# Optimization experiments

Hardware: AMD Instinct MI355X
Metric: run time of the kernel (lower is better)

Reference implementation:

```python
import jax, jax.numpy as jnp
import numpy as np

B, S, D, H, E = 4, 2048, 512, 8, 4  # batch, seq, embed, heads, expand
HD = D // H


def setup_inputs() -> dict:
    key = jax.random.key(0)
    ks = jax.random.split(key, 9)
    s = lambda k, shape, fan: jax.random.normal(k, shape, jnp.float32) * (fan ** -0.5)
    return {
        "x": jax.random.normal(ks[0], (B, S, D), jnp.float32),
        "Wq": s(ks[1], (D, D), D),
        "Wk": s(ks[2], (D, D), D),
        "Wv": s(ks[3], (D, D), D),
        "Wo": s(ks[4], (D, D), D),
        "W1": s(ks[5], (D, D * E), D),
        "b1": jnp.zeros((D * E,), jnp.float32),
        "W2": s(ks[6], (D * E, D), D * E),
        "b2": jnp.zeros((D,), jnp.float32),
    }


def _encoder_layer(x, Wq, Wk, Wv, Wo, W1, b1, W2, b2):
    # NOTE: source computes InstanceNorm1d twice but discards both results -> no-ops.
    scale = D ** -0.25  # applied to BOTH q and k (net 1/sqrt(embed_dim))
    q = (x @ Wq).reshape(B, S, H, HD).transpose(0, 2, 1, 3) * scale  # [B,H,S,hd]
    k = (x @ Wk).reshape(B, S, H, HD).transpose(0, 2, 1, 3) * scale
    v = (x @ Wv).reshape(B, S, H, HD).transpose(0, 2, 1, 3)
    scores = jnp.einsum('bhqd,bhkd->bhqk', q, k)  # [B,H,S,S]
    attn = jax.nn.softmax(scores, axis=-1)
    o = jnp.einsum('bhqk,bhkd->bhqd', attn, v)  # [B,H,S,hd]
    o = o.transpose(0, 2, 1, 3).reshape(B, S, D)
    x = o @ Wo + x  # residual 1
    h = jax.nn.gelu(x @ W1 + b1, approximate=True)  # torch GELU(approximate='tanh')
    return h @ W2 + b2 + x  # residual 2 (dropout=0, eval)


def reference(x, Wq, Wk, Wv, Wo, W1, b1, W2, b2):
    return _encoder_layer(x, Wq, Wk, Wv, Wo, W1, b1, W2, b2)
```

## Files before the change

kernel.cpp:

```cpp
#include <hip/hip_runtime.h>
#include <hip/hip_bf16.h>


typedef __bf16 bf16;
typedef __attribute__((ext_vector_type(8))) __bf16 bf16x8;
typedef __attribute__((ext_vector_type(4))) __bf16 bf16x4;
typedef __attribute__((ext_vector_type(4))) float f32x4;
typedef __attribute__((ext_vector_type(16))) float f32x16;
typedef __attribute__((ext_vector_type(2))) unsigned int u32x2;
typedef __attribute__((ext_vector_type(4))) unsigned int u32x4;

#define LOG2E 1.4426950408889634f
#define SCORE_SCALE 0.044194173824159216f
#define SCALE_L2E (SCORE_SCALE * LOG2E)

#if __has_builtin(__builtin_amdgcn_exp2f)
#define EXP2(x) __builtin_amdgcn_exp2f(x)
#else
#define EXP2(x) exp2f(x)
#endif

__device__ __forceinline__ void gl_lds16(const bf16* g, bf16* l) {
  __builtin_amdgcn_global_load_lds(
      (const __attribute__((address_space(1))) unsigned int*)g,
      (__attribute__((address_space(3))) unsigned int*)l, 16, 0, 0);
}

template <int N>
__device__ __forceinline__ void wait_vm_barrier() {
  if constexpr (N == 0)
    asm volatile("s_waitcnt vmcnt(0)\ns_barrier" ::: "memory");
  else if constexpr (N == 2)
    asm volatile("s_waitcnt vmcnt(2)\ns_barrier" ::: "memory");
  else if constexpr (N == 3)
    asm volatile("s_waitcnt vmcnt(3)\ns_barrier" ::: "memory");
  else if constexpr (N == 4)
    asm volatile("s_waitcnt vmcnt(4)\ns_barrier" ::: "memory");
  else if constexpr (N == 8)
    asm volatile("s_waitcnt vmcnt(8)\ns_barrier" ::: "memory");
}

__device__ __forceinline__ float gelu_tanh(float x) {
  float u = 0.7978845608028654f * (x + 0.044715f * x * x * x);
  float e = EXP2(u * (2.0f * LOG2E));
  float th = 1.0f - 2.0f / (e + 1.0f);
  return 0.5f * x * (1.0f + th);
}

__device__ __forceinline__ f32x4 mfma_bf16(bf16x8 a, bf16x8 b, f32x4 c) {
  return __builtin_amdgcn_mfma_f32_16x16x32_bf16(a, b, c, 0, 0, 0);
}
__device__ __forceinline__ f32x16 mfma32x16(bf16x8 a, bf16x8 b, f32x16 c) {
  return __builtin_amdgcn_mfma_f32_32x32x16_bf16(a, b, c, 0, 0, 0);
}

__device__ __forceinline__ void plswap(unsigned int& a, unsigned int& b) {
  asm volatile("v_permlane32_swap_b32 %0, %1" : "+v"(a), "+v"(b));
}

__device__ __forceinline__ void xcd_remap(int& bx, int& by) {
  const int gx = gridDim.x;
  const int nwg = gx * gridDim.y;
  const int lin = blockIdx.y * gx + blockIdx.x;
  const int id = (lin & 7) * (nwg >> 3) + (lin >> 3);
  bx = id % gx;
  by = id / gx;
}

template <int MODE, typename OutT, int TN>
__global__ __launch_bounds__(256, 2) void gemm_bt(
    const bf16* __restrict__ A, const bf16* __restrict__ Bt,
    OutT* __restrict__ C, const float* __restrict__ bias,
    const float* __restrict__ resf, const bf16* __restrict__ resb,
    bf16* __restrict__ vt, int M, int N, int K) {
  constexpr int MI = (TN == 128) ? 4 : 2;
  constexpr int NBUF = (TN == 128) ? 2 : 3;
  __shared__ __align__(16) bf16 sA[NBUF][128 * 32];
  __shared__ __align__(16) bf16 sB[NBUF][TN * 32];
  const int tid = threadIdx.x;
  const int lane = tid & 63;
  const int quad = lane >> 4, lc = lane & 15;
  const int wave = tid >> 6;
  const int wr = (TN == 128) ? (wave >> 1) : wave;
  const int wc = (TN == 128) ? (wave & 1) : 0;
  int bxs, bys;
  xcd_remap(bxs, bys);
  const int m0 = bys * 128, n0 = bxs * TN;

  const int srow = tid >> 2;
  const int kc = (tid & 3) * 8;
  const bf16* Ag1 = A + (size_t)(m0 + srow) * K + kc;
  const bf16* Ag2 = A + (size_t)(m0 + 64 + srow) * K + kc;
  const bf16* Bg1 = Bt + (size_t)(n0 + srow) * K + kc;
  const bf16* Bg2 = Bt + (size_t)(n0 + 64 + srow) * K + kc;
  const int o1 = tid * 8, o2 = (tid + 256) * 8;

  f32x4 acc[MI][4];
#pragma unroll
  for (int mi = 0; mi < MI; ++mi)
#pragma unroll
    for (int ni = 0; ni < 4; ++ni) acc[mi][ni] = (f32x4){0.f, 0.f, 0.f, 0.f};

  const int kIters = K >> 5;

  if constexpr (TN == 128) {
    gl_lds16(Ag1, sA[0] + o1);
    gl_lds16(Ag2, sA[0] + o2);
    gl_lds16(Bg1, sB[0] + o1);
    gl_lds16(Bg2, sB[0] + o2);
    Ag1 += 32; Ag2 += 32; Bg1 += 32; Bg2 += 32;

    for (int kt = 0; kt < kIters; ++kt) {
      __syncthreads();
      const bf16* cA = sA[kt & 1];
      const bf16* cB = sB[kt & 1];
      if (kt + 1 < kIters) {
        bf16* nA = sA[(kt + 1) & 1];
        bf16* nB = sB[(kt + 1) & 1];
        gl_lds16(Ag1, nA + o1);
        gl_lds16(Ag2, nA + o2);
        gl_lds16(Bg1, nB + o1);
        gl_lds16(Bg2, nB + o2);
        Ag1 += 32; Ag2 += 32; Bg1 += 32; Bg2 += 32;
      }
      bf16x8 af[MI], bfm[4];
#pragma unroll
      for (int i = 0; i < MI; ++i)
        af[i] = *(const bf16x8*)(cA +
                                 ((wr * 64 + i * 16 + lc) * 32 + quad * 8));
#pragma unroll
      for (int i = 0; i < 4; ++i)
        bfm[i] =
            *(const bf16x8*)(cB + ((wc * 64 + i * 16 + lc) * 32 + quad * 8));
#pragma unroll
      for (int mi = 0; mi < MI; ++mi)
#pragma unroll
        for (int ni = 0; ni < 4; ++ni)
          acc[mi][ni] = mfma_bf16(af[mi], bfm[ni], acc[mi][ni]);
    }
  } else {
    auto stage = [&](int t) {
      bf16* a = sA[t % 3];
      bf16* bb = sB[t % 3];
      gl_lds16(Ag1 + t * 32, a + o1);
      gl_lds16(Ag2 + t * 32, a + o2);
      gl_lds16(Bg1 + t * 32, bb + o1);
    };
    stage(0);
    stage(1);
    for (int kt = 0; kt < kIters; ++kt) {
      if (kt + 1 < kIters)
        wait_vm_barrier<3>();
      else
        wait_vm_barrier<0>();
      if (kt + 2 < kIters) stage(kt + 2);
      const bf16* cA = sA[kt % 3];
      const bf16* cB = sB[kt % 3];
      bf16x8 af[MI], bfm[4];
#pragma unroll
      for (int i = 0; i < MI; ++i)
        af[i] = *(const bf16x8*)(cA +
                                 ((wr * 32 + i * 16 + lc) * 32 + quad * 8));
#pragma unroll
      for (int i = 0; i < 4; ++i)
        bfm[i] = *(const bf16x8*)(cB + ((i * 16 + lc) * 32 + quad * 8));
#pragma unroll
      for (int mi = 0; mi < MI; ++mi)
#pragma unroll
        for (int ni = 0; ni < 4; ++ni)
          acc[mi][ni] = mfma_bf16(af[mi], bfm[ni], acc[mi][ni]);
    }
  }

  if constexpr (MODE == 0) {
    if (n0 >= 1024) {
#pragma unroll
      for (int mi = 0; mi < MI; ++mi) {
        const int row0 = m0 + wr * (16 * MI) + mi * 16 + quad * 4;
        const int bb = row0 >> 11, s0 = row0 & 2047;
#pragma unroll
        for (int ni = 0; ni < 4; ++ni) {
          const int col = n0 + wc * 64 + ni * 16 + lc;
          const int hh = (col >> 6) & 7, d = col & 63;
          bf16x4 pb;
#pragma unroll
          for (int r = 0; r < 4; ++r) pb[r] = (bf16)acc[mi][ni][r];
          *(bf16x4*)(vt + ((size_t)((bb * 8 + hh) * 64 + d)) * 2048 + s0) = pb;
        }
      }
      return;
    }
  }
  const float qscale = (MODE == 0 && n0 < 512) ? SCALE_L2E : 1.0f;
#pragma unroll
  for (int mi = 0; mi < MI; ++mi) {
#pragma unroll
    for (int r = 0; r < 4; ++r) {
      const int row = m0 + wr * (16 * MI) + mi * 16 + quad * 4 + r;
#pragma unroll
      for (int ni = 0; ni < 4; ++ni) {
        const int col = n0 + wc * 64 + ni * 16 + lc;
        const size_t idx = (size_t)row * N + col;
        float v = acc[mi][ni][r];
        if (MODE == 0) v *= qscale;
        if (MODE == 1) v += resf[idx];
        if (MODE == 2) v = gelu_tanh(v + bias[col]);
        if (MODE == 3) v += bias[col] + (float)resb[idx];
        C[idx] = (OutT)v;
      }
    }
  }
}

__global__ __launch_bounds__(512, 2) void gemm256v2(
    const bf16* __restrict__ A, const bf16* __restrict__ Bt,
    bf16* __restrict__ C, const float* __restrict__ bias, int M, int N,
    int K) {
  __shared__ __align__(16) bf16 sA[4][8192];
  __shared__ __align__(16) bf16 sB[4][8192];
  const int tid = threadIdx.x;
  const int lane = tid & 63;
  const int quad = lane >> 4, lc = lane & 15;
  const int w8 = tid >> 6;
  const int wm = w8 >> 2, wn = w8 & 3;
  int bxs, bys;
  xcd_remap(bxs, bys);
  const int m0 = bys * 256, n0 = bxs * 256;

  const int srow0 = tid >> 2;
  const int cpos = tid & 3;

  f32x4 acc[8][4];
#pragma unroll
  for (int mi = 0; mi < 8; ++mi)
#pragma unroll
    for (int ni = 0; ni < 4; ++ni) acc[mi][ni] = (f32x4){0.f, 0.f, 0.f, 0.f};

  auto stage = [&](int t) {
    bf16* a = sA[t & 3];
    bf16* bb = sB[t & 3];
    const int k0 = t * 32;
#pragma unroll
    for (int c = 0; c < 2; ++c) {
      const int row = c * 128 + srow0;
      const int sc = (cpos ^ (row & 3)) * 8;
      gl_lds16(A + (size_t)(m0 + row) * K + k0 + sc, a + c * 4096 + tid * 8);
      gl_lds16(Bt + (size_t)(n0 + row) * K + k0 + sc, bb + c * 4096 + tid * 8);
    }
  };

  const int kIters = K >> 5;
  stage(0);
  stage(1);
  stage(2);

  const int cxq = (quad ^ (lc & 3)) << 3;

  for (int kt = 0; kt < kIters; ++kt) {
    const int left = kIters - 1 - kt;
    if (left >= 2)
      wait_vm_barrier<8>();
    else if (left == 1)
      wait_vm_barrier<4>();
    else
      wait_vm_barrier<0>();
    if (kt + 3 < kIters) stage(kt + 3);
    const bf16* cA = sA[kt & 3];
    const bf16* cB = sB[kt & 3];

    bf16x8 af[8], bfm[4];
#pragma unroll
    for (int i = 0; i < 4; ++i)
      af[i] = *(const bf16x8*)(cA + (wm * 128 + i * 16 + lc) * 32 + cxq);
#pragma unroll
    for (int j = 0; j < 4; ++j)
      bfm[j] = *(const bf16x8*)(cB + (wn * 64 + j * 16 + lc) * 32 + cxq);
    __builtin_amdgcn_s_barrier();
    __builtin_amdgcn_s_setprio(1);
#pragma unroll
    for (int mi = 0; mi < 4; ++mi)
#pragma unroll
      for (int ni = 0; ni < 4; ++ni)
        acc[mi][ni] = mfma_bf16(af[mi], bfm[ni], acc[mi][ni]);
    __builtin_amdgcn_s_setprio(0);
#pragma unroll
    for (int i = 4; i < 8; ++i)
      af[i] = *(const bf16x8*)(cA + (wm * 128 + i * 16 + lc) * 32 + cxq);
    __builtin_amdgcn_s_barrier();
    __builtin_amdgcn_s_setprio(1);
#pragma unroll
    for (int mi = 4; mi < 8; ++mi)
#pragma unroll
      for (int ni = 0; ni < 4; ++ni)
        acc[mi][ni] = mfma_bf16(af[mi], bfm[ni], acc[mi][ni]);
    __builtin_amdgcn_s_setprio(0);
  }

#pragma unroll
  for (int mi = 0; mi < 8; ++mi) {
#pragma unroll
    for (int r = 0; r < 4; ++r) {
      const int row = m0 + wm * 128 + mi * 16 + quad * 4 + r;
#pragma unroll
      for (int ni = 0; ni < 4; ++ni) {
        const int col = n0 + wn * 64 + ni * 16 + lc;
        C[(size_t)row * N + col] = (bf16)gelu_tanh(acc[mi][ni][r] + bias[col]);
      }
    }
  }
}

__global__ __launch_bounds__(256, 4) void flash_attn(
    const bf16* __restrict__ QKV, const bf16* __restrict__ Vt,
    float* __restrict__ O0, float* __restrict__ O1, float* __restrict__ Rp) {
  const int tid = threadIdx.x;
  const int lane = tid & 63, wave = tid >> 6;
  const int lo5 = lane & 31, hi = lane >> 5;
  const int lin = blockIdx.y * 16 + blockIdx.x;
  const int xcd = lin & 7, slot = lin >> 3;
  const int bh = xcd * 4 + (slot >> 4);
  const int qt = slot & 15;
  const int b = bh >> 3, h = bh & 7;
  const int q0 = qt * 128 + wave * 32;
  const int half = blockIdx.z;
  const int t0 = half << 4;

  __shared__ __align__(16) bf16 sK[3][4096];
  __shared__ __align__(16) bf16 sV[2][4096];

  const bf16* Qrow = QKV + (size_t)(b * 2048 + q0 + lo5) * 1536 + h * 64;
  bf16x8 qf[4];
#pragma unroll
  for (int i = 0; i < 4; ++i) qf[i] = *(const bf16x8*)(Qrow + i * 16 + hi * 8);

  const int colsw = (((lane & 7) ^ (lane >> 3)) << 3);
  const bf16* Kg0 = QKV + (size_t)b * 2048 * 1536 + 512 + (size_t)h * 64 +
                    (size_t)(wave * 16 + (lane >> 3)) * 1536 + colsw;
  const bf16* Vg0 = Vt + (size_t)bh * 64 * 2048 +
                    (size_t)(wave * 16 + (lane >> 3)) * 2048 + colsw;
  const int stag = wave * 1024;
  const int m7 = lo5 & 7;

  f32x16 oacc[2];
  oacc[0] = (f32x16)(0.f);
  oacc[1] = (f32x16)(0.f);
  float rs0 = 0.f, rs1 = 0.f, rs2 = 0.f, rs3 = 0.f;

  auto stageK = [&](int lt) {
    bf16* dk = sK[lt % 3] + stag;
    const int g = t0 + lt;
    gl_lds16(Kg0 + (size_t)g * 64 * 1536, dk);
    gl_lds16(Kg0 + (size_t)(g * 64 + 8) * 1536, dk + 512);
  };
  auto stageV = [&](int lt) {
    bf16* dv = sV[lt & 1] + stag;
    const int g = t0 + lt;
    gl_lds16(Vg0 + g * 64, dv);
    gl_lds16(Vg0 + g * 64 + 8 * 2048, dv + 512);
  };
  stageK(0);
  stageV(0);
  stageK(1);

  bf16x8 paw[4];

  auto softmax = [&](const f32x16& st, int hl) {
    unsigned int q32[4][2];
#pragma unroll
    for (int g = 0; g < 4; ++g) {
      bf16x4 pb;
      float p0 = EXP2(st[4 * g + 0]);
      float p1 = EXP2(st[4 * g + 1]);
      float p2 = EXP2(st[4 * g + 2]);
      float p3 = EXP2(st[4 * g + 3]);
      rs0 += p0; rs1 += p1; rs2 += p2; rs3 += p3;
      pb[0] = (bf16)p0; pb[1] = (bf16)p1; pb[2] = (bf16)p2; pb[3] = (bf16)p3;
      u32x2 w2 = __builtin_bit_cast(u32x2, pb);
      q32[g][0] = w2[0];
      q32[g][1] = w2[1];
    }
#pragma unroll
    for (int t = 0; t < 2; ++t) {
      unsigned int a0 = q32[2 * t][0], a1 = q32[2 * t][1];
      unsigned int b0 = q32[2 * t + 1][0], b1 = q32[2 * t + 1][1];
      plswap(a0, b0);
      plswap(a1, b1);
      u32x4 f = {a0, a1, b0, b1};
      paw[hl * 2 + t] = __builtin_bit_cast(bf16x8, f);
    }
  };

  for (int kt = 0; kt < 16; ++kt) {
    if (kt == 15)
      wait_vm_barrier<0>();
    else
      wait_vm_barrier<2>();
    if (kt + 1 < 16) stageV(kt + 1);
    if (kt + 2 < 16) stageK(kt + 2);
    const bf16* cK = sK[kt % 3];
    const bf16* cV = sV[kt & 1];

    bf16x8 vf[2][4], kf[2][4];
#pragma unroll
    for (int dh = 0; dh < 2; ++dh) {
      const int Rd = dh * 32 + lo5;
#pragma unroll
      for (int w = 0; w < 4; ++w)
        vf[dh][w] =
            *(const bf16x8*)(cV + Rd * 64 + (((2 * w + hi) ^ m7) << 3));
    }
#pragma unroll
    for (int hl = 0; hl < 2; ++hl) {
      const int R = hl * 32 + lo5;
#pragma unroll
      for (int i = 0; i < 4; ++i)
        kf[hl][i] =
            *(const bf16x8*)(cK + R * 64 + (((2 * i + hi) ^ m7) << 3));
    }

    f32x16 st0 = (f32x16)(0.f), st1 = (f32x16)(0.f);
    __builtin_amdgcn_s_setprio(1);
#pragma unroll
    for (int i = 0; i < 4; ++i) {
      st0 = mfma32x16(kf[0][i], qf[i], st0);
      st1 = mfma32x16(kf[1][i], qf[i], st1);
    }
    __builtin_amdgcn_s_setprio(0);

    softmax(st0, 0);
#pragma unroll
    for (int w = 0; w < 2; ++w) {
      oacc[0] = mfma32x16(paw[w], vf[0][w], oacc[0]);
      oacc[1] = mfma32x16(paw[w], vf[1][w], oacc[1]);
    }
    softmax(st1, 1);
    __builtin_amdgcn_s_setprio(1);
#pragma unroll
    for (int w = 2; w < 4; ++w) {
      oacc[0] = mfma32x16(paw[w], vf[0][w], oacc[0]);
      oacc[1] = mfma32x16(paw[w], vf[1][w], oacc[1]);
    }
    __builtin_amdgcn_s_setprio(0);
  }

  float rsum = (rs0 + rs1) + (rs2 + rs3);
  rsum += __shfl_xor(rsum, 32, 64);
  float* Op = half ? O1 : O0;
  const size_t obase = (size_t)(b * 2048 + q0) * 512 + h * 64;
#pragma unroll
  for (int r = 0; r < 16; ++r) {
    const int qloc = (r & 3) + 8 * (r >> 2) + 4 * hi;
#pragma unroll
    for (int dh = 0; dh < 2; ++dh)
      Op[obase + (size_t)qloc * 512 + dh * 32 + lo5] = oacc[dh][r];
  }
  if (hi == 0)
    Rp[(size_t)(half * 8 + h) * 8192 + b * 2048 + q0 + lo5] = rsum;
}

__global__ __launch_bounds__(256) void combine(
    const float* __restrict__ O0, const float* __restrict__ O1,
    const float* __restrict__ Rp, bf16* __restrict__ attn) {
  const int i4 = blockIdx.x * 256 + threadIdx.x;
  const int row = i4 >> 7;
  const int col = (i4 & 127) * 4;
  const int h = col >> 6;
  const float inv =
      1.0f / (Rp[(size_t)h * 8192 + row] + Rp[(size_t)(8 + h) * 8192 + row]);
  const float4 a = ((const float4*)O0)[i4];
  const float4 b = ((const float4*)O1)[i4];
  bf16x4 o;
  o[0] = (bf16)((a.x + b.x) * inv);
  o[1] = (bf16)((a.y + b.y) * inv);
  o[2] = (bf16)((a.z + b.z) * inv);
  o[3] = (bf16)((a.w + b.w) * inv);
  *(bf16x4*)(attn + (size_t)i4 * 4) = o;
}

__global__ __launch_bounds__(256) void prep(
    const float* __restrict__ x, const float* __restrict__ Wq,
    const float* __restrict__ Wk, const float* __restrict__ Wv,
    const float* __restrict__ Wo, const float* __restrict__ W1,
    const float* __restrict__ W2, bf16* __restrict__ xb,
    bf16* __restrict__ WqkvT, bf16* __restrict__ WoT, bf16* __restrict__ W1T,
    bf16* __restrict__ W2T) {
  const int bid = blockIdx.x;
  if (bid < 4096) {
    const size_t i = ((size_t)bid * 256 + threadIdx.x) * 4;
    const float4 v = *(const float4*)(x + i);
    bf16x4 o;
    o[0] = (bf16)v.x; o[1] = (bf16)v.y; o[2] = (bf16)v.z; o[3] = (bf16)v.w;
    *(bf16x4*)(xb + i) = o;
    return;
  }
  const int t = bid - 4096;
  const float* in;
  bf16* out;
  int in_ld, out_ld, bx, by;
  if (t < 1024) {
    const int q = t >> 8, r = t & 255;
    bx = r & 15; by = r >> 4; in_ld = 512; out_ld = 512;
    in = (q == 0) ? Wq : (q == 1) ? Wk : (q == 2) ? Wv : Wo;
    out = (q == 0) ? WqkvT
          : (q == 1) ? WqkvT + 512 * 512
          : (q == 2) ? WqkvT + 2 * 512 * 512
                     : WoT;
  } else if (t < 2048) {
    const int r = t - 1024;
    bx = r & 63; by = r >> 6; in_ld = 2048; out_ld = 512;
    in = W1; out = W1T;
  } else {
    const int r = t - 2048;
    bx = r & 15; by = r >> 4; in_ld = 512; out_ld = 2048;
    in = W2; out = W2T;
  }
  __shared__ __align__(16) bf16 tl[32][33];
  const int tx = threadIdx.x & 31, ty = threadIdx.x >> 5;
  const int n0 = bx * 32, k0 = by * 32;
#pragma unroll
  for (int i = 0; i < 4; ++i)
    tl[ty + 8 * i][tx] = (bf16)in[(size_t)(k0 + ty + 8 * i) * in_ld + n0 + tx];
  __syncthreads();
#pragma unroll
  for (int i = 0; i < 4; ++i)
    out[(size_t)(n0 + ty + 8 * i) * out_ld + k0 + tx] = tl[tx][ty + 8 * i];
}

extern "C" void kernel_launch(void* const* d_in, const int* in_sizes, int n_in,
                              void* d_out, int out_size, void* d_ws,
                              size_t ws_size, hipStream_t stream) {
  const float* x = (const float*)d_in[0];
  const float* Wq = (const float*)d_in[1];
  const float* Wk = (const float*)d_in[2];
  const float* Wv = (const float*)d_in[3];
  const float* Wo = (const float*)d_in[4];
  const float* W1 = (const float*)d_in[5];
  const float* b1 = (const float*)d_in[6];
  const float* W2 = (const float*)d_in[7];
  const float* b2 = (const float*)d_in[8];
  float* out = (float*)d_out;

  char* ws = (char*)d_ws;
  size_t off = 0;
  auto alloc = [&](size_t bytes) {
    char* p = ws + off;
    off += (bytes + 255) & ~(size_t)255;
    return p;
  };
  bf16* WqkvT = (bf16*)alloc(1536ULL * 512 * 2);
  bf16* WoT = (bf16*)alloc(512ULL * 512 * 2);
  bf16* W1T = (bf16*)alloc(2048ULL * 512 * 2);
  bf16* W2T = (bf16*)alloc(512ULL * 2048 * 2);
  bf16* xb = (bf16*)alloc(8192ULL * 512 * 2);
  bf16* QKV = (bf16*)alloc(8192ULL * 1536 * 2);
  bf16* Vt = (bf16*)alloc(32ULL * 64 * 2048 * 2);
  bf16* attn = (bf16*)alloc(8192ULL * 512 * 2);
  float* Opart1 = (float*)alloc(8192ULL * 512 * 4);
  float* Rpart = (float*)alloc(2ULL * 8 * 8192 * 4);
  float* Opart0 = out;
  bf16* x2 = xb;
  bf16* hbuf = QKV;

  const dim3 tb(256);
  prep<<<dim3(7168), tb, 0, stream>>>(x, Wq, Wk, Wv, Wo, W1, W2, xb, WqkvT,
                                      WoT, W1T, W2T);
  gemm_bt<0, bf16, 128><<<dim3(12, 64), tb, 0, stream>>>(
      xb, WqkvT, QKV, nullptr, nullptr, nullptr, Vt, 8192, 1536, 512);
  flash_attn<<<dim3(16, 32, 2), tb, 0, stream>>>(QKV, Vt, Opart0, Opart1,
                                                 Rpart);
  combine<<<dim3(4096), tb, 0, stream>>>(Opart0, Opart1, Rpart, attn);
  gemm_bt<1, bf16, 64><<<dim3(8, 64), tb, 0, stream>>>(
      attn, WoT, x2, nullptr, x, nullptr, nullptr, 8192, 512, 512);
  gemm256v2<<<dim3(8, 32), dim3(512), 0, stream>>>(x2, W1T, hbuf, b1, 8192,
                                                   2048, 512);
  gemm_bt<3, float, 64><<<dim3(8, 64), tb, 0, stream>>>(
      hbuf, W2T, out, b2, nullptr, x2, nullptr, 8192, 512, 2048);
}
```

Baseline: 285.0 us.

## Merge split-KV attention halves into one block and reduce through LDS

```diff
diff --git a/kernel.cpp b/kernel.cpp
--- a/kernel.cpp
+++ b/kernel.cpp
@@ -310,23 +310,23 @@
   }
 }
 
-__global__ __launch_bounds__(256, 4) void flash_attn(
+__global__ __launch_bounds__(512, 2) void flash_attn(
     const bf16* __restrict__ QKV, const bf16* __restrict__ Vt,
-    float* __restrict__ O0, float* __restrict__ O1, float* __restrict__ Rp) {
+    bf16* __restrict__ O) {
   const int tid = threadIdx.x;
   const int lane = tid & 63, wave = tid >> 6;
+  const int hs = wave >> 2, w4 = wave & 3;
   const int lo5 = lane & 31, hi = lane >> 5;
   const int lin = blockIdx.y * 16 + blockIdx.x;
   const int xcd = lin & 7, slot = lin >> 3;
   const int bh = xcd * 4 + (slot >> 4);
   const int qt = slot & 15;
   const int b = bh >> 3, h = bh & 7;
-  const int q0 = qt * 128 + wave * 32;
-  const int half = blockIdx.z;
-  const int t0 = half << 4;
-
-  __shared__ __align__(16) bf16 sK[3][4096];
-  __shared__ __align__(16) bf16 sV[2][4096];
+  const int q0 = qt * 128 + w4 * 32;
+  const int t0 = hs << 4;
+
+  __shared__ __align__(16) bf16 sK[2][3][4096];
+  __shared__ __align__(16) bf16 sV[2][2][4096];
 
   const bf16* Qrow = QKV + (size_t)(b * 2048 + q0 + lo5) * 1536 + h * 64;
   bf16x8 qf[4];
@@ -335,10 +335,10 @@
 
   const int colsw = (((lane & 7) ^ (lane >> 3)) << 3);
   const bf16* Kg0 = QKV + (size_t)b * 2048 * 1536 + 512 + (size_t)h * 64 +
-                    (size_t)(wave * 16 + (lane >> 3)) * 1536 + colsw;
+                    (size_t)(w4 * 16 + (lane >> 3)) * 1536 + colsw;
   const bf16* Vg0 = Vt + (size_t)bh * 64 * 2048 +
-                    (size_t)(wave * 16 + (lane >> 3)) * 2048 + colsw;
-  const int stag = wave * 1024;
+                    (size_t)(w4 * 16 + (lane >> 3)) * 2048 + colsw;
+  const int stag = w4 * 1024;
   const int m7 = lo5 & 7;
 
   f32x16 oacc[2];
@@ -347,13 +347,13 @@
   float rs0 = 0.f, rs1 = 0.f, rs2 = 0.f, rs3 = 0.f;
 
   auto stageK = [&](int lt) {
-    bf16* dk = sK[lt % 3] + stag;
+    bf16* dk = sK[hs][lt % 3] + stag;
     const int g = t0 + lt;
     gl_lds16(Kg0 + (size_t)g * 64 * 1536, dk);
     gl_lds16(Kg0 + (size_t)(g * 64 + 8) * 1536, dk + 512);
   };
   auto stageV = [&](int lt) {
-    bf16* dv = sV[lt & 1] + stag;
+    bf16* dv = sV[hs][lt & 1] + stag;
     const int g = t0 + lt;
     gl_lds16(Vg0 + g * 64, dv);
     gl_lds16(Vg0 + g * 64 + 8 * 2048, dv + 512);
@@ -397,8 +397,8 @@
       wait_vm_barrier<2>();
     if (kt + 1 < 16) stageV(kt + 1);
     if (kt + 2 < 16) stageK(kt + 2);
-    const bf16* cK = sK[kt % 3];
-    const bf16* cV = sV[kt & 1];
+    const bf16* cK = sK[hs][kt % 3];
+    const bf16* cV = sV[hs][kt & 1];
 
     bf16x8 vf[2][4], kf[2][4];
 #pragma unroll
@@ -445,36 +445,34 @@
 
   float rsum = (rs0 + rs1) + (rs2 + rs3);
   rsum += __shfl_xor(rsum, 32, 64);
-  float* Op = half ? O1 : O0;
-  const size_t obase = (size_t)(b * 2048 + q0) * 512 + h * 64;
-#pragma unroll
-  for (int r = 0; r < 16; ++r) {
-    const int qloc = (r & 3) + 8 * (r >> 2) + 4 * hi;
+
+  __syncthreads();
+  float* cb = (float*)(&sK[0][0][0]);
+  float* cr = cb + 8192;
+  if (hs == 1) {
 #pragma unroll
     for (int dh = 0; dh < 2; ++dh)
-      Op[obase + (size_t)qloc * 512 + dh * 32 + lo5] = oacc[dh][r];
-  }
-  if (hi == 0)
-    Rp[(size_t)(half * 8 + h) * 8192 + b * 2048 + q0 + lo5] = rsum;
-}
-
-__global__ __launch_bounds__(256) void combine(
-    const float* __restrict__ O0, const float* __restrict__ O1,
-    const float* __restrict__ Rp, bf16* __restrict__ attn) {
-  const int i4 = blockIdx.x * 256 + threadIdx.x;
-  const int row = i4 >> 7;
-  const int col = (i4 & 127) * 4;
-  const int h = col >> 6;
-  const float inv =
-      1.0f / (Rp[(size_t)h * 8192 + row] + Rp[(size_t)(8 + h) * 8192 + row]);
-  const float4 a = ((const float4*)O0)[i4];
-  const float4 b = ((const float4*)O1)[i4];
-  bf16x4 o;
-  o[0] = (bf16)((a.x + b.x) * inv);
-  o[1] = (bf16)((a.y + b.y) * inv);
-  o[2] = (bf16)((a.z + b.z) * inv);
-  o[3] = (bf16)((a.w + b.w) * inv);
-  *(bf16x4*)(attn + (size_t)i4 * 4) = o;
+#pragma unroll
+      for (int r = 0; r < 16; ++r)
+        cb[((w4 * 2 + dh) * 16 + r) * 64 + lane] = oacc[dh][r];
+    if (hi == 0) cr[w4 * 32 + lo5] = rsum;
+  }
+  __syncthreads();
+  if (hs == 0) {
+    const float rtot = rsum + cr[w4 * 32 + lo5];
+    const size_t obase = (size_t)(b * 2048 + q0) * 512 + h * 64;
+#pragma unroll
+    for (int r = 0; r < 16; ++r) {
+      const int qloc = (r & 3) + 8 * (r >> 2) + 4 * hi;
+      const float inv = 1.0f / __shfl(rtot, qloc, 64);
+#pragma unroll
+      for (int dh = 0; dh < 2; ++dh) {
+        const float v =
+            oacc[dh][r] + cb[((w4 * 2 + dh) * 16 + r) * 64 + lane];
+        O[obase + (size_t)qloc * 512 + dh * 32 + lo5] = (bf16)(v * inv);
+      }
+    }
+  }
 }
 
 __global__ __launch_bounds__(256) void prep(
@@ -555,9 +553,6 @@
   bf16* QKV = (bf16*)alloc(8192ULL * 1536 * 2);
   bf16* Vt = (bf16*)alloc(32ULL * 64 * 2048 * 2);
   bf16* attn = (bf16*)alloc(8192ULL * 512 * 2);
-  float* Opart1 = (float*)alloc(8192ULL * 512 * 4);
-  float* Rpart = (float*)alloc(2ULL * 8 * 8192 * 4);
-  float* Opart0 = out;
   bf16* x2 = xb;
   bf16* hbuf = QKV;
 
@@ -566,9 +561,7 @@
                                       WoT, W1T, W2T);
   gemm_bt<0, bf16, 128><<<dim3(12, 64), tb, 0, stream>>>(
       xb, WqkvT, QKV, nullptr, nullptr, nullptr, Vt, 8192, 1536, 512);
-  flash_attn<<<dim3(16, 32, 2), tb, 0, stream>>>(QKV, Vt, Opart0, Opart1,
-                                                 Rpart);
-  combine<<<dim3(4096), tb, 0, stream>>>(Opart0, Opart1, Rpart, attn);
+  flash_attn<<<dim3(16, 32), dim3(512), 0, stream>>>(QKV, Vt, attn);
   gemm_bt<1, bf16, 64><<<dim3(8, 64), tb, 0, stream>>>(
       attn, WoT, x2, nullptr, x, nullptr, nullptr, 8192, 512, 512);
   gemm256v2<<<dim3(8, 32), dim3(512), 0, stream>>>(x2, W1T, hbuf, b1, 8192,
```

New measurement: 253.3 us. 1.13x faster.
